# Kernel tuning notes

Hardware: AMD Instinct MI355X
Metric: run time of the kernel (lower is better)

## Reference

```python
import jax, jax.numpy as jnp
import numpy as np

DIM = 64
N_EMBED = 1024


def setup_inputs() -> dict:
    key = jax.random.key(0)
    k1, k2 = jax.random.split(key)
    input = jax.random.normal(k1, (32, 64, 64, DIM), dtype=jnp.float32)
    embed = jax.random.normal(k2, (DIM, N_EMBED), dtype=jnp.float32)
    return {"input": input, "embed": embed}


def reference(input, embed):
    # Flatten all leading dims: [N, dim]
    flatten = input.reshape(-1, DIM)
    # Squared L2 distance to each code: [N, n_embed]
    dist = (
        jnp.sum(flatten * flatten, axis=1, keepdims=True)
        - 2.0 * (flatten @ embed)
        + jnp.sum(embed * embed, axis=0, keepdims=True)
    )
    embed_ind_flat = jnp.argmin(dist, axis=1)  # argmax(-dist)
    embed_ind = embed_ind_flat.reshape(input.shape[:-1])
    # Codebook lookup: embed.T is [n_embed, dim]
    quantize = jnp.take(embed.T, embed_ind, axis=0)  # [..., dim]
    # Commitment loss with detached quantize
    diff = jnp.mean((jax.lax.stop_gradient(quantize) - input) ** 2)
    # Straight-through estimator
    quantize = input + jax.lax.stop_gradient(quantize - input)
    num_used_codebooks = -1  # eval-mode constant, as in the torch module
    return quantize, diff, embed_ind, num_used_codebooks
```

## Files before the change

### kernel.cpp

```cpp
#include <hip/hip_runtime.h>
#include <hip/hip_bf16.h>

#define DIM      64
#define NCODE    1024
#define NROWS    131072
#define NTILES   64
#define TAU      0.006f
#define TSTRIDE  4160

typedef __attribute__((ext_vector_type(8))) short  short8;
typedef __attribute__((ext_vector_type(4))) float  f32x4;

#define DIFF_OFF 8388608
#define IND_OFF  8388609
#define NU_OFF   (8388609 + 131072)

#define WS_HEE      0
#define WS_EMBEDT   1024
#define WS_PARTIALS 66560
#define WS_PIDX     67072
#define WS_COUNTER  198144
#define WS_FLAGLIST 198145
#define WS_BPK      329220

__device__ __forceinline__ unsigned short bf16rn(float f) {
    unsigned int u = __float_as_uint(f);
    return (unsigned short)((u + 0x7FFFu + ((u >> 16) & 1u)) >> 16);
}
__device__ __forceinline__ float bf16tof(unsigned short h) {
    return __uint_as_float(((unsigned int)h) << 16);
}
__device__ __forceinline__ unsigned umin_(unsigned a, unsigned b) { return a < b ? a : b; }
__device__ __forceinline__ unsigned umax_(unsigned a, unsigned b) { return a > b ? a : b; }

__global__ __launch_bounds__(256) void vq_prep(const float* __restrict__ embed,
                                               float* __restrict__ embedT,
                                               float* __restrict__ hee,
                                               int* __restrict__ counter,
                                               unsigned char* __restrict__ bpk) {
    if (blockIdx.x < 4) {
        int c = blockIdx.x * 256 + threadIdx.x;
        if (c == 0) *counter = 0;
        float s = 0.f;
#pragma unroll
        for (int d = 0; d < DIM; ++d) {
            float v = embed[d * NCODE + c];
            embedT[c * DIM + d] = v;
            s = fmaf(v, v, s);
        }
        hee[c] = 0.5f * s;
    } else {
        int t  = (blockIdx.x - 4) * 256 + threadIdx.x;
        int s  = t & 1;
        int l  = (t >> 1) & 63;
        int ct = t >> 7;
        int c  = ct * 16 + (l & 15);
        int kb = s * 32 + (l >> 4) * 8;

        unsigned int hw[4], lw[4];
#pragma unroll
        for (int w = 0; w < 4; ++w) {
            float v0 = embed[(kb + 2 * w)     * NCODE + c];
            float v1 = embed[(kb + 2 * w + 1) * NCODE + c];
            unsigned short h0 = bf16rn(v0), h1 = bf16rn(v1);
            unsigned short l0 = bf16rn(v0 - bf16tof(h0));
            unsigned short l1 = bf16rn(v1 - bf16tof(h1));
            hw[w] = (unsigned int)h0 | ((unsigned int)h1 << 16);
            lw[w] = (unsigned int)l0 | ((unsigned int)l1 << 16);
        }
        uint4* dst_h = (uint4*)(bpk + ct * TSTRIDE + 64 + s * 1024 + l * 16);
        uint4* dst_l = (uint4*)(bpk + ct * TSTRIDE + 64 + s * 1024 + l * 16 + 2048);
        *dst_h = make_uint4(hw[0], hw[1], hw[2], hw[3]);
        *dst_l = make_uint4(lw[0], lw[1], lw[2], lw[3]);
        if (s == 0 && l < 16) {
            float ss = 0.f;
#pragma unroll
            for (int d = 0; d < DIM; ++d) {
                float v = embed[d * NCODE + c];
                ss = fmaf(v, v, ss);
            }
            *(float*)(bpk + ct * TSTRIDE + l * 4) = 0.5f * ss;
        }
    }
}

__global__ __launch_bounds__(256, 4) void vq_score_mfma(const float* __restrict__ input,
                                                        const unsigned char* __restrict__ bpk,
                                                        float* __restrict__ pidx,
                                                        int* __restrict__ counter,
                                                        int* __restrict__ flaglist) {
    const int tid   = threadIdx.x;
    const int wid   = tid >> 6;
    const int lane  = tid & 63;
    const int g     = lane >> 4;
    const int lc    = lane & 15;
    const int rbase = (blockIdx.x * 4 + wid) * 32;

    short8 ah[2][2], al[2][2];
    float  hx[2][4];
#pragma unroll
    for (int m = 0; m < 2; ++m) {
        float ssum = 0.f;
#pragma unroll
        for (int s = 0; s < 2; ++s) {
            const float* xr = input + (size_t)(rbase + m * 16 + lc) * DIM + s * 32 + g * 8;
            float4 f0 = *(const float4*)(xr);
            float4 f1 = *(const float4*)(xr + 4);
            float xf[8] = {f0.x, f0.y, f0.z, f0.w, f1.x, f1.y, f1.z, f1.w};
            short8 h8, l8;
#pragma unroll
            for (int j = 0; j < 8; ++j) {
                ssum = fmaf(xf[j], xf[j], ssum);
                float nx = -xf[j];
                unsigned short hb = bf16rn(nx);
                h8[j] = (short)hb;
                l8[j] = (short)bf16rn(nx - bf16tof(hb));
            }
            ah[m][s] = h8;
            al[m][s] = l8;
        }
        ssum += __shfl_xor(ssum, 16, 64);
        ssum += __shfl_xor(ssum, 32, 64);
#pragma unroll
        for (int j = 0; j < 4; ++j)
            hx[m][j] = 0.5f * __shfl(ssum, g * 4 + j, 64) + 1.0f;
    }

    unsigned m1[8], m2[8];
#pragma unroll
    for (int t = 0; t < 8; ++t) { m1[t] = 0xFFFFFFFFu; m2[t] = 0xFFFFFFFFu; }

    const unsigned char* fb = bpk + lane * 16 + 64;
    const unsigned char* hb = bpk + lc * 4;

#define LOADT(T, C0, C1, C2, C3, HH)                                          \
    {   const unsigned char* tp = fb + (T) * TSTRIDE;                         \
        C0 = *(const short8*)(tp);                                            \
        C1 = *(const short8*)(tp + 1024);                                     \
        C2 = *(const short8*)(tp + 2048);                                     \
        C3 = *(const short8*)(tp + 3072);                                     \
        HH = *(const float*)(hb + (T) * TSTRIDE); }

#define COMPT(T, C0, C1, C2, C3, HH)                                          \
    {   _Pragma("unroll")                                                     \
        for (int m = 0; m < 2; ++m) {                                         \
            f32x4 acc = {HH + hx[m][0], HH + hx[m][1],                        \
                         HH + hx[m][2], HH + hx[m][3]};                       \
            acc = __builtin_amdgcn_mfma_f32_16x16x32_bf16(ah[m][0], C0, acc, 0, 0, 0); \
            acc = __builtin_amdgcn_mfma_f32_16x16x32_bf16(al[m][0], C0, acc, 0, 0, 0); \
            acc = __builtin_amdgcn_mfma_f32_16x16x32_bf16(ah[m][0], C2, acc, 0, 0, 0); \
            acc = __builtin_amdgcn_mfma_f32_16x16x32_bf16(ah[m][1], C1, acc, 0, 0, 0); \
            acc = __builtin_amdgcn_mfma_f32_16x16x32_bf16(al[m][1], C1, acc, 0, 0, 0); \
            acc = __builtin_amdgcn_mfma_f32_16x16x32_bf16(ah[m][1], C3, acc, 0, 0, 0); \
            _Pragma("unroll")                                                 \
            for (int j = 0; j < 4; ++j) {                                     \
                unsigned bits = __float_as_uint(acc[j]);                      \
                unsigned pk   = (bits & 0xFFFFFFC0u) | (unsigned)(T);         \
                int s = m * 4 + j;                                            \
                m2[s] = umin_(m2[s], umax_(pk, m1[s]));                       \
                m1[s] = umin_(m1[s], pk);                                     \
            }                                                                 \
        } }

    short8 a0, a1, a2, a3;  float ahh;
    short8 b0, b1, b2, b3;  float bhh;

    LOADT(0, a0, a1, a2, a3, ahh);
    for (int ct = 0; ct < NTILES - 2; ct += 2) {
        LOADT(ct + 1, b0, b1, b2, b3, bhh);
        COMPT(ct, a0, a1, a2, a3, ahh);
        LOADT(ct + 2, a0, a1, a2, a3, ahh);
        COMPT(ct + 1, b0, b1, b2, b3, bhh);
    }
    LOADT(NTILES - 1, b0, b1, b2, b3, bhh);
    COMPT(NTILES - 2, a0, a1, a2, a3, ahh);
    COMPT(NTILES - 1, b0, b1, b2, b3, bhh);

#undef LOADT
#undef COMPT

#pragma unroll
    for (int m = 0; m < 2; ++m) {
#pragma unroll
        for (int j = 0; j < 4; ++j) {
            int s = m * 4 + j;
            unsigned v1 = m1[s], v2 = m2[s];
            int ii = (int)(((v1 & 63u) << 4) | (unsigned)lc);
#pragma unroll
            for (int d = 1; d < 16; d <<= 1) {
                unsigned o1 = __shfl_xor(v1, d, 64);
                int      oi = __shfl_xor(ii, d, 64);
                unsigned o2 = __shfl_xor(v2, d, 64);
                bool sw = (o1 < v1) || (o1 == v1 && oi < ii);
                unsigned losing = sw ? v1 : o1;
                v2 = umin_(umin_(v2, o2), losing);
                v1 = sw ? o1 : v1;
                ii = sw ? oi : ii;
            }
            if (lc == 0) {
                int r = rbase + m * 16 + g * 4 + j;
                pidx[r] = (float)ii;
                float gap = __uint_as_float(v2 & 0xFFFFFFC0u)
                          - __uint_as_float(v1 & 0xFFFFFFC0u);
                if (gap < TAU) {
                    int p = atomicAdd(counter, 1);
                    flaglist[p] = r;
                }
            }
        }
    }
}

__global__ __launch_bounds__(64) void vq_rescore(const float* __restrict__ input,
                                                 const float* __restrict__ embedT,
                                                 const float* __restrict__ hee,
                                                 const int* __restrict__ counter,
                                                 const int* __restrict__ flaglist,
                                                 float* __restrict__ pidx) {
    const int lane = threadIdx.x;
    const int cnt  = *counter;
    for (int i = blockIdx.x * 2; i < cnt; i += gridDim.x * 2) {
        const int r0 = flaglist[i];
        const int r1 = (i + 1 < cnt) ? flaglist[i + 1] : r0;
        float4 xa[16], xb[16];
        {
            const float4* pa = (const float4*)(input + (size_t)r0 * DIM);
            const float4* pb = (const float4*)(input + (size_t)r1 * DIM);
#pragma unroll
            for (int k = 0; k < 16; ++k) { xa[k] = pa[k]; xb[k] = pb[k]; }
        }
        float bestA = -3.402823466e+38f, bestB = -3.402823466e+38f;
        int   biA = 0, biB = 0;
#pragma unroll 1
        for (int k = 0; k < 16; ++k) {
            int c = lane * 16 + k;
            const float4* e4 = (const float4*)(embedT + (size_t)c * DIM);
            float hh = hee[c];
            float a0 = -hh, a1 = 0.f, a2 = 0.f, a3 = 0.f;
            float b0 = -hh, b1 = 0.f, b2 = 0.f, b3 = 0.f;
#pragma unroll
            for (int q = 0; q < 4; ++q) {
                float4 e0 = e4[4 * q + 0], e1 = e4[4 * q + 1];
                float4 e2 = e4[4 * q + 2], e3 = e4[4 * q + 3];
                float4 p0 = xa[4 * q + 0], p1 = xa[4 * q + 1];
                float4 p2 = xa[4 * q + 2], p3 = xa[4 * q + 3];
                float4 q0 = xb[4 * q + 0], q1 = xb[4 * q + 1];
                float4 q2 = xb[4 * q + 2], q3 = xb[4 * q + 3];
                a0 = fmaf(e0.x, p0.x, a0); a0 = fmaf(e0.y, p0.y, a0);
                a0 = fmaf(e0.z, p0.z, a0); a0 = fmaf(e0.w, p0.w, a0);
                a1 = fmaf(e1.x, p1.x, a1); a1 = fmaf(e1.y, p1.y, a1);
                a1 = fmaf(e1.z, p1.z, a1); a1 = fmaf(e1.w, p1.w, a1);
                a2 = fmaf(e2.x, p2.x, a2); a2 = fmaf(e2.y, p2.y, a2);
                a2 = fmaf(e2.z, p2.z, a2); a2 = fmaf(e2.w, p2.w, a2);
                a3 = fmaf(e3.x, p3.x, a3); a3 = fmaf(e3.y, p3.y, a3);
                a3 = fmaf(e3.z, p3.z, a3); a3 = fmaf(e3.w, p3.w, a3);
                b0 = fmaf(e0.x, q0.x, b0); b0 = fmaf(e0.y, q0.y, b0);
                b0 = fmaf(e0.z, q0.z, b0); b0 = fmaf(e0.w, q0.w, b0);
                b1 = fmaf(e1.x, q1.x, b1); b1 = fmaf(e1.y, q1.y, b1);
                b1 = fmaf(e1.z, q1.z, b1); b1 = fmaf(e1.w, q1.w, b1);
                b2 = fmaf(e2.x, q2.x, b2); b2 = fmaf(e2.y, q2.y, b2);
                b2 = fmaf(e2.z, q2.z, b2); b2 = fmaf(e2.w, q2.w, b2);
                b3 = fmaf(e3.x, q3.x, b3); b3 = fmaf(e3.y, q3.y, b3);
                b3 = fmaf(e3.z, q3.z, b3); b3 = fmaf(e3.w, q3.w, b3);
            }
            float sA = (a0 + a1) + (a2 + a3);
            float sB = (b0 + b1) + (b2 + b3);
            if (sA > bestA) { bestA = sA; biA = c; }
            if (sB > bestB) { bestB = sB; biB = c; }
        }
#pragma unroll
        for (int d = 1; d < 64; d <<= 1) {
            float oA = __shfl_xor(bestA, d, 64);
            int   iA = __shfl_xor(biA, d, 64);
            bool  sA = (oA > bestA) || (oA == bestA && iA < biA);
            bestA = sA ? oA : bestA;
            biA   = sA ? iA : biA;
            float oB = __shfl_xor(bestB, d, 64);
            int   iB = __shfl_xor(biB, d, 64);
            bool  sB = (oB > bestB) || (oB == bestB && iB < biB);
            bestB = sB ? oB : bestB;
            biB   = sB ? iB : biB;
        }
        if (lane == 0) {
            pidx[r0] = (float)biA;
            pidx[r1] = (float)biB;
        }
    }
}

__global__ __launch_bounds__(256) void vq_combine(const float* __restrict__ input,
                                                  const float* __restrict__ embedT,
                                                  const float* __restrict__ pidx,
                                                  float* __restrict__ out_q,
                                                  float* __restrict__ out_ind,
                                                  float* __restrict__ partials) {
    __shared__ float wsum[4];
    const int tid = threadIdx.x;
    const int r   = blockIdx.x * 256 + tid;

    int bi = (int)pidx[r];
    out_ind[r] = (float)bi;

    float acc = 0.f;
    {
        const float4* x4 = (const float4*)(input + (size_t)r * DIM);
        const float4* q4 = (const float4*)(embedT + (size_t)bi * DIM);
        float4* o4 = (float4*)(out_q + (size_t)r * DIM);
#pragma unroll
        for (int k = 0; k < 16; ++k) {
            float4 q = q4[k];
            float4 x = x4[k];
            o4[k] = q;
            float dx = q.x - x.x; acc = fmaf(dx, dx, acc);
            dx = q.y - x.y;       acc = fmaf(dx, dx, acc);
            dx = q.z - x.z;       acc = fmaf(dx, dx, acc);
            dx = q.w - x.w;       acc = fmaf(dx, dx, acc);
        }
    }
#pragma unroll
    for (int off = 32; off > 0; off >>= 1) acc += __shfl_down(acc, off, 64);
    if ((tid & 63) == 0) wsum[tid >> 6] = acc;
    __syncthreads();
    if (tid == 0) partials[blockIdx.x] = (wsum[0] + wsum[1]) + (wsum[2] + wsum[3]);
}

__global__ __launch_bounds__(256) void vq_finalize(const float* __restrict__ partials,
                                                   float* __restrict__ out,
                                                   int out_size) {
    __shared__ float sm[256];
    int t = threadIdx.x;
    float v = partials[t] + partials[t + 256];
    sm[t] = v;
    __syncthreads();
    for (int s = 128; s > 0; s >>= 1) {
        if (t < s) sm[t] += sm[t + s];
        __syncthreads();
    }
    if (t == 0) out[DIFF_OFF] = sm[0] / 8388608.0f;
    if (t == 1 && out_size > NU_OFF) out[NU_OFF] = -1.0f;
}

extern "C" void kernel_launch(void* const* d_in, const int* in_sizes, int n_in,
                              void* d_out, int out_size, void* d_ws, size_t ws_size,
                              hipStream_t stream) {
    const float* input = (const float*)d_in[0];
    const float* embed = (const float*)d_in[1];
    float* out = (float*)d_out;
    float* ws  = (float*)d_ws;

    float* hee      = ws + WS_HEE;
    float* embedT   = ws + WS_EMBEDT;
    float* partials = ws + WS_PARTIALS;
    float* pidx     = ws + WS_PIDX;
    int*   counter  = (int*)(ws + WS_COUNTER);
    int*   flaglist = (int*)(ws + WS_FLAGLIST);
    unsigned char* bpk = (unsigned char*)(ws + WS_BPK);

    vq_prep<<<36, 256, 0, stream>>>(embed, embedT, hee, counter, bpk);
    vq_score_mfma<<<1024, 256, 0, stream>>>(input, bpk, pidx, counter, flaglist);
    vq_rescore<<<2048, 64, 0, stream>>>(input, embedT, hee, counter, flaglist, pidx);
    vq_combine<<<512, 256, 0, stream>>>(input, embedT, pidx,
                                        out, out + IND_OFF, partials);
    vq_finalize<<<1, 256, 0, stream>>>(partials, out, out_size);
}
```

Measured before the change: 113.1 us.

## Stage codebook tiles into LDS via global_load_lds double buffering

Codebook tiles were previously loaded redundantly by every wave straight from global memory into registers. Now each wave copies a quarter of each 4 KB tile into a shared double-buffered LDS area using direct global-to-LDS loads, and all waves then read the tile from LDS. This cuts global/L2 traffic by a factor of four per block. In exchange it adds two block-wide barriers per tile pair and LDS reads, and the correctness of the overlap depends on the barrier placement being sufficient for the asynchronous LDS writes.

```diff
diff --git a/kernel.cpp b/kernel.cpp
--- a/kernel.cpp
+++ b/kernel.cpp
@@ -32,6 +32,13 @@
 }
 __device__ __forceinline__ unsigned umin_(unsigned a, unsigned b) { return a < b ? a : b; }
 __device__ __forceinline__ unsigned umax_(unsigned a, unsigned b) { return a > b ? a : b; }
+
+__device__ __forceinline__ void stage16(const void* gsrc, void* ldst) {
+    __builtin_amdgcn_global_load_lds(
+        (const __attribute__((address_space(1))) unsigned int*)gsrc,
+        (__attribute__((address_space(3))) unsigned int*)ldst,
+        16, 0, 0);
+}
 
 __global__ __launch_bounds__(256) void vq_prep(const float* __restrict__ embed,
                                                float* __restrict__ embedT,
@@ -89,6 +96,8 @@
                                                         float* __restrict__ pidx,
                                                         int* __restrict__ counter,
                                                         int* __restrict__ flaglist) {
+    __shared__ __align__(16) unsigned char ltile[2 * 4096];
+
     const int tid   = threadIdx.x;
     const int wid   = tid >> 6;
     const int lane  = tid & 63;
@@ -130,22 +139,22 @@
 #pragma unroll
     for (int t = 0; t < 8; ++t) { m1[t] = 0xFFFFFFFFu; m2[t] = 0xFFFFFFFFu; }
 
-    const unsigned char* fb = bpk + lane * 16 + 64;
-    const unsigned char* hb = bpk + lc * 4;
-
-#define LOADT(T, C0, C1, C2, C3, HH)                                          \
-    {   const unsigned char* tp = fb + (T) * TSTRIDE;                         \
-        C0 = *(const short8*)(tp);                                            \
-        C1 = *(const short8*)(tp + 1024);                                     \
-        C2 = *(const short8*)(tp + 2048);                                     \
-        C3 = *(const short8*)(tp + 3072);                                     \
-        HH = *(const float*)(hb + (T) * TSTRIDE); }
-
-#define COMPT(T, C0, C1, C2, C3, HH)                                          \
-    {   _Pragma("unroll")                                                     \
+#define STAGE(T, BOFF)                                                        \
+    stage16(bpk + (size_t)(T) * TSTRIDE + 64 + wid * 1024 + lane * 16,        \
+            ltile + (BOFF) + wid * 1024);
+
+#define HEEG(T) (*(const float*)(bpk + (size_t)(T) * TSTRIDE + lc * 4))
+
+#define COMPT(T, BOFF, HH)                                                    \
+    {   const unsigned char* lb = ltile + (BOFF) + lane * 16;                 \
+        short8 C0 = *(const short8*)(lb);                                     \
+        short8 C1 = *(const short8*)(lb + 1024);                              \
+        short8 C2 = *(const short8*)(lb + 2048);                              \
+        short8 C3 = *(const short8*)(lb + 3072);                              \
+        _Pragma("unroll")                                                     \
         for (int m = 0; m < 2; ++m) {                                         \
-            f32x4 acc = {HH + hx[m][0], HH + hx[m][1],                        \
-                         HH + hx[m][2], HH + hx[m][3]};                       \
+            f32x4 acc = {(HH) + hx[m][0], (HH) + hx[m][1],                    \
+                         (HH) + hx[m][2], (HH) + hx[m][3]};                   \
             acc = __builtin_amdgcn_mfma_f32_16x16x32_bf16(ah[m][0], C0, acc, 0, 0, 0); \
             acc = __builtin_amdgcn_mfma_f32_16x16x32_bf16(al[m][0], C0, acc, 0, 0, 0); \
             acc = __builtin_amdgcn_mfma_f32_16x16x32_bf16(ah[m][0], C2, acc, 0, 0, 0); \
@@ -162,21 +171,28 @@
             }                                                                 \
         } }
 
-    short8 a0, a1, a2, a3;  float ahh;
-    short8 b0, b1, b2, b3;  float bhh;
-
-    LOADT(0, a0, a1, a2, a3, ahh);
+    STAGE(0, 0);
+    float hhA = HEEG(0);
+    __syncthreads();
+
     for (int ct = 0; ct < NTILES - 2; ct += 2) {
-        LOADT(ct + 1, b0, b1, b2, b3, bhh);
-        COMPT(ct, a0, a1, a2, a3, ahh);
-        LOADT(ct + 2, a0, a1, a2, a3, ahh);
-        COMPT(ct + 1, b0, b1, b2, b3, bhh);
-    }
-    LOADT(NTILES - 1, b0, b1, b2, b3, bhh);
-    COMPT(NTILES - 2, a0, a1, a2, a3, ahh);
-    COMPT(NTILES - 1, b0, b1, b2, b3, bhh);
-
-#undef LOADT
+        STAGE(ct + 1, 4096);
+        float hhB = HEEG(ct + 1);
+        COMPT(ct, 0, hhA);
+        __syncthreads();
+        STAGE(ct + 2, 0);
+        hhA = HEEG(ct + 2);
+        COMPT(ct + 1, 4096, hhB);
+        __syncthreads();
+    }
+    STAGE(NTILES - 1, 4096);
+    float hhB = HEEG(NTILES - 1);
+    COMPT(NTILES - 2, 0, hhA);
+    __syncthreads();
+    COMPT(NTILES - 1, 4096, hhB);
+
+#undef STAGE
+#undef HEEG
 #undef COMPT
 
 #pragma unroll
```

New measurement: 112.1 us. Within noise of the previous version (-0.8%).
